# Optimization experiments

Measured on AMD Instinct MI355X. Metric: run time of the kernel, lower is better.

The kernel has to match this reference:

```python
import jax, jax.numpy as jnp
import numpy as np


def _filter_flow(img, filters, K):
    # img: [N, 2, H, W]; filters: [N, K*K, H, W] per-pixel adaptive kernels
    N, C, H, W = img.shape
    pad = (K - 1) // 2
    imgp = jnp.pad(img, ((0, 0), (0, 0), (pad, pad), (pad, pad)))
    # patches: [N, C*K*K, H, W], channel-major then row-major (dy, dx) --
    # matches torch F.unfold per single channel
    patches = jax.lax.conv_general_dilated_patches(
        imgp, (K, K), (1, 1), 'VALID',
        dimension_numbers=('NCHW', 'OIHW', 'NCHW'))
    patches = patches.reshape(N, C, K * K, H, W)
    return jnp.sum(patches * filters[:, None], axis=2)  # [N, 2, H, W]


def _grid(N, H, W, dtype):
    xx = jnp.broadcast_to(jnp.arange(W, dtype=dtype)[None, :], (H, W)) / max(W - 1, 1)
    yy = jnp.broadcast_to(jnp.arange(H, dtype=dtype)[:, None], (H, W)) / max(H - 1, 1)
    return jnp.broadcast_to(jnp.stack([xx, yy])[None], (N, 2, H, W))


def setup_inputs() -> dict:
    key = jax.random.key(0)
    k1, k2 = jax.random.split(key)
    N, K, H, W = 4, 11, 256, 256
    FF_AtoB = jax.random.uniform(k1, (N, K * K, H, W), dtype=jnp.float32)
    FF_BtoA = jax.random.uniform(k2, (N, K * K, H, W), dtype=jnp.float32)
    return {"FF_AtoB": FF_AtoB, "FF_BtoA": FF_BtoA, "filter_size": K}


def reference(FF_AtoB, FF_BtoA, filter_size):
    weight = 1.0
    N, C, H, W = FF_AtoB.shape
    K = filter_size
    grid = _grid(N, H, W, FF_AtoB.dtype)

    def cycle_loss(ff1, ff2):
        m = _filter_flow(grid, ff1, K)
        m = _filter_flow(m, ff2, K)
        diff = jnp.sqrt(jnp.sum((grid - m) ** 2, axis=1))  # [N, H, W]
        per_img = jnp.sum(diff, axis=(1, 2)) / (H * W)
        return jnp.sum(per_img) / N

    loss_ABA = cycle_loss(FF_AtoB, FF_BtoA)
    loss_BAB = cycle_loss(FF_BtoA, FF_AtoB)
    return (loss_ABA + loss_BAB) * weight
```

## Files before the change

kernel.cpp:

```cpp
#include <hip/hip_runtime.h>
#include <math.h>

#define NB   4
#define KF   11
#define KK   121
#define HH   256
#define WW   256
#define HW   (HH * WW)
#define PADK 5
#define TW   (WW + 2 * PADK)
#define INVD (1.0f / 255.0f)

__global__ __launch_bounds__(256) void pass1_kernel(const float* __restrict__ F,
                                                    float* __restrict__ m1) {
    const int n = blockIdx.x / HH;
    const int h = blockIdx.x % HH;
    const int w = threadIdx.x;

    const float* fp = F + (size_t)n * KK * HW + h * WW + w;

    float xv[KF], mk[KF];
#pragma unroll
    for (int kx = 0; kx < KF; ++kx) {
        int cc = w + kx - PADK;
        bool ok = (cc >= 0 && cc < WW);
        xv[kx] = ok ? (float)cc * INVD : 0.0f;
        mk[kx] = ok ? 1.0f : 0.0f;
    }

    float ax = 0.0f, ay = 0.0f;
    for (int ky = 0; ky < KF; ++ky) {
        int rr = h + ky - PADK;
        if (rr < 0 || rr >= HH) continue;
        float yv = (float)rr * INVD;
        const float* fr = fp + (size_t)ky * KF * HW;
        float srow = 0.0f;
#pragma unroll
        for (int kx = 0; kx < KF; ++kx) {
            float f = fr[(size_t)kx * HW];
            ax = fmaf(f, xv[kx], ax);
            srow = fmaf(f, mk[kx], srow);
        }
        ay = fmaf(yv, srow, ay);
    }

    size_t o = (size_t)n * 2 * HW + h * WW + w;
    m1[o] = ax;
    m1[o + HW] = ay;
}

template <bool FUSE>
__global__ __launch_bounds__(256) void pass2_kernel(const float* __restrict__ F,
                                                    const float* __restrict__ m1in,
                                                    float* __restrict__ m1out,
                                                    float* __restrict__ acc) {
    __shared__ float tile[2 * KF * TW];
    __shared__ float wsum[4];

    const int n = blockIdx.x / HH;
    const int h = blockIdx.x % HH;
    const int w = threadIdx.x;

    const float* mbase = m1in + (size_t)n * 2 * HW;
    for (int t = threadIdx.x; t < 2 * KF * TW; t += 256) {
        int ch = t / (KF * TW);
        int rem = t - ch * (KF * TW);
        int r = rem / TW;
        int c = rem - r * TW;
        int rr = h + r - PADK;
        int cc = c - PADK;
        float v = 0.0f;
        if (rr >= 0 && rr < HH && cc >= 0 && cc < WW)
            v = mbase[(size_t)ch * HW + rr * WW + cc];
        tile[t] = v;
    }
    __syncthreads();

    const float* fp = F + (size_t)n * KK * HW + h * WW + w;

    float xv[KF], mk[KF];
#pragma unroll
    for (int kx = 0; kx < KF; ++kx) {
        int cc = w + kx - PADK;
        bool ok = (cc >= 0 && cc < WW);
        xv[kx] = ok ? (float)cc * INVD : 0.0f;
        mk[kx] = ok ? 1.0f : 0.0f;
    }

    float a1x = 0.0f, a1y = 0.0f;
    float a2x = 0.0f, a2y = 0.0f;

    for (int ky = 0; ky < KF; ++ky) {
        int rr = h + ky - PADK;
        if (rr < 0 || rr >= HH) continue;
        float yv = (float)rr * INVD;
        const float* fr = fp + (size_t)ky * KF * HW;
        const float* t0 = tile + ky * TW + w;
        const float* t1 = t0 + KF * TW;
        float srow = 0.0f;
#pragma unroll
        for (int kx = 0; kx < KF; ++kx) {
            float f = fr[(size_t)kx * HW];
            if (FUSE) {
                a1x = fmaf(f, xv[kx], a1x);
                srow = fmaf(f, mk[kx], srow);
            }
            a2x = fmaf(f, t0[kx], a2x);
            a2y = fmaf(f, t1[kx], a2y);
        }
        if (FUSE) a1y = fmaf(yv, srow, a1y);
    }

    if (FUSE) {
        size_t o = (size_t)n * 2 * HW + h * WW + w;
        m1out[o] = a1x;
        m1out[o + HW] = a1y;
    }

    float gx = (float)w * INVD, gy = (float)h * INVD;
    float dx = gx - a2x, dy = gy - a2y;
    float d = sqrtf(dx * dx + dy * dy);

#pragma unroll
    for (int off = 32; off > 0; off >>= 1) d += __shfl_down(d, off, 64);
    int lane = threadIdx.x & 63, wid = threadIdx.x >> 6;
    if (lane == 0) wsum[wid] = d;
    __syncthreads();
    if (threadIdx.x == 0) atomicAdd(acc, wsum[0] + wsum[1] + wsum[2] + wsum[3]);
}

__global__ void finalize_kernel(const float* __restrict__ acc, float* __restrict__ out) {
    out[0] = (acc[0] + acc[1]) * (1.0f / ((float)HW * (float)NB));
}

extern "C" void kernel_launch(void* const* d_in, const int* in_sizes, int n_in,
                              void* d_out, int out_size, void* d_ws, size_t ws_size,
                              hipStream_t stream) {
    const float* FA = (const float*)d_in[0];
    const float* FB = (const float*)d_in[1];
    float* out = (float*)d_out;

    float* m1A = (float*)d_ws;
    float* m1B = m1A + (size_t)NB * 2 * HW;
    float* acc = m1B + (size_t)NB * 2 * HW;

    hipMemsetAsync(acc, 0, 2 * sizeof(float), stream);

    dim3 grid(NB * HH), block(256);
    pass1_kernel<<<grid, block, 0, stream>>>(FA, m1A);
    pass2_kernel<true><<<grid, block, 0, stream>>>(FB, m1A, m1B, acc);
    pass2_kernel<false><<<grid, block, 0, stream>>>(FA, m1B, nullptr, acc + 1);

    finalize_kernel<<<1, 1, 0, stream>>>(acc, out);
}
```

Baseline: 309.7 us.

## Process two pixels per thread and two rows per block with float2 loads

Each thread now computes two adjacent pixels using float2 loads of the filter planes, and each block covers two output rows, sharing one 12-row halo tile in shared memory. Tile values are loaded into registers once per row and reused across both pixels, so there are fewer LDS reads and wider global loads. Atomic accumulation is replaced by per-block partial sums that a 256-thread finalize kernel reduces, which also removes the memset. Register pressure goes up and the grid shrinks by half.

```diff
diff --git a/kernel.cpp b/kernel.cpp
--- a/kernel.cpp
+++ b/kernel.cpp
@@ -1,136 +1,179 @@
 #include <hip/hip_runtime.h>
 #include <math.h>
 
-#define NB   4
-#define KF   11
-#define KK   121
-#define HH   256
-#define WW   256
-#define HW   (HH * WW)
-#define PADK 5
-#define TW   (WW + 2 * PADK)
-#define INVD (1.0f / 255.0f)
+#define NB    4
+#define KF    11
+#define KK    121
+#define HH    256
+#define WW    256
+#define HW    (HH * WW)
+#define PADK  5
+#define TROWS 12
+#define TW2   268
+#define INVD  (1.0f / 255.0f)
+#define RPB   2
+#define GRID1 (NB * HH / RPB)
 
 __global__ __launch_bounds__(256) void pass1_kernel(const float* __restrict__ F,
                                                     float* __restrict__ m1) {
-    const int n = blockIdx.x / HH;
-    const int h = blockIdx.x % HH;
-    const int w = threadIdx.x;
+    const int t   = threadIdx.x;
+    const int n   = blockIdx.x / (HH / RPB);
+    const int h0  = (blockIdx.x % (HH / RPB)) * RPB;
+    const int sub = t >> 7;
+    const int j   = t & 127;
+    const int h   = h0 + sub;
+    const int w0  = j * 2;
 
-    const float* fp = F + (size_t)n * KK * HW + h * WW + w;
+    const float2* fp = (const float2*)(F + (size_t)n * KK * HW + (size_t)h * WW + w0);
 
-    float xv[KF], mk[KF];
+    float mk0[KF], mk1[KF];
 #pragma unroll
     for (int kx = 0; kx < KF; ++kx) {
-        int cc = w + kx - PADK;
-        bool ok = (cc >= 0 && cc < WW);
-        xv[kx] = ok ? (float)cc * INVD : 0.0f;
-        mk[kx] = ok ? 1.0f : 0.0f;
+        int c0 = w0 + kx - PADK;
+        mk0[kx] = (c0 >= 0 && c0 < WW) ? 1.0f : 0.0f;
+        mk1[kx] = (c0 + 1 >= 0 && c0 + 1 < WW) ? 1.0f : 0.0f;
     }
+    const float b0 = (float)(w0 - PADK) * INVD;
 
-    float ax = 0.0f, ay = 0.0f;
+    float ax0 = 0, ay0 = 0, ax1 = 0, ay1 = 0;
     for (int ky = 0; ky < KF; ++ky) {
         int rr = h + ky - PADK;
         if (rr < 0 || rr >= HH) continue;
         float yv = (float)rr * INVD;
-        const float* fr = fp + (size_t)ky * KF * HW;
-        float srow = 0.0f;
+        const float2* fr = fp + (size_t)(ky * KF) * (HW / 2);
+        float s0 = 0, s1 = 0;
 #pragma unroll
         for (int kx = 0; kx < KF; ++kx) {
-            float f = fr[(size_t)kx * HW];
-            ax = fmaf(f, xv[kx], ax);
-            srow = fmaf(f, mk[kx], srow);
+            float2 f = fr[(size_t)kx * (HW / 2)];
+            float u0 = f.x * mk0[kx], u1 = f.y * mk1[kx];
+            float xk = b0 + (float)kx * INVD;
+            ax0 = fmaf(u0, xk, ax0);
+            ax1 = fmaf(u1, xk + INVD, ax1);
+            s0 += u0; s1 += u1;
         }
-        ay = fmaf(yv, srow, ay);
+        ay0 = fmaf(yv, s0, ay0);
+        ay1 = fmaf(yv, s1, ay1);
     }
-
-    size_t o = (size_t)n * 2 * HW + h * WW + w;
-    m1[o] = ax;
-    m1[o + HW] = ay;
+    float2* ox = (float2*)(m1 + (size_t)n * 2 * HW + (size_t)h * WW + w0);
+    float2* oy = (float2*)(m1 + (size_t)n * 2 * HW + HW + (size_t)h * WW + w0);
+    *ox = make_float2(ax0, ax1);
+    *oy = make_float2(ay0, ay1);
 }
 
 template <bool FUSE>
 __global__ __launch_bounds__(256) void pass2_kernel(const float* __restrict__ F,
                                                     const float* __restrict__ m1in,
                                                     float* __restrict__ m1out,
-                                                    float* __restrict__ acc) {
-    __shared__ float tile[2 * KF * TW];
+                                                    float* __restrict__ partial) {
+    __shared__ float tile[2 * TROWS * TW2];
     __shared__ float wsum[4];
 
-    const int n = blockIdx.x / HH;
-    const int h = blockIdx.x % HH;
-    const int w = threadIdx.x;
+    const int t   = threadIdx.x;
+    const int n   = blockIdx.x / (HH / RPB);
+    const int h0  = (blockIdx.x % (HH / RPB)) * RPB;
+    const int sub = t >> 7;
+    const int j   = t & 127;
+    const int h   = h0 + sub;
+    const int w0  = j * 2;
 
     const float* mbase = m1in + (size_t)n * 2 * HW;
-    for (int t = threadIdx.x; t < 2 * KF * TW; t += 256) {
-        int ch = t / (KF * TW);
-        int rem = t - ch * (KF * TW);
-        int r = rem / TW;
-        int c = rem - r * TW;
-        int rr = h + r - PADK;
-        int cc = c - PADK;
+    for (int i = t; i < 2 * TROWS * TW2; i += 256) {
+        int ch  = i / (TROWS * TW2);
+        int rem = i - ch * (TROWS * TW2);
+        int r   = rem / TW2;
+        int c   = rem - r * TW2;
+        int rr  = h0 + r - PADK;
+        int cc  = c - PADK;
         float v = 0.0f;
         if (rr >= 0 && rr < HH && cc >= 0 && cc < WW)
             v = mbase[(size_t)ch * HW + rr * WW + cc];
-        tile[t] = v;
+        tile[i] = v;
     }
     __syncthreads();
 
-    const float* fp = F + (size_t)n * KK * HW + h * WW + w;
+    const float2* fp = (const float2*)(F + (size_t)n * KK * HW + (size_t)h * WW + w0);
 
-    float xv[KF], mk[KF];
+    float mk0[KF], mk1[KF];
 #pragma unroll
     for (int kx = 0; kx < KF; ++kx) {
-        int cc = w + kx - PADK;
-        bool ok = (cc >= 0 && cc < WW);
-        xv[kx] = ok ? (float)cc * INVD : 0.0f;
-        mk[kx] = ok ? 1.0f : 0.0f;
+        int c0 = w0 + kx - PADK;
+        mk0[kx] = (c0 >= 0 && c0 < WW) ? 1.0f : 0.0f;
+        mk1[kx] = (c0 + 1 >= 0 && c0 + 1 < WW) ? 1.0f : 0.0f;
     }
+    const float b0 = (float)(w0 - PADK) * INVD;
 
-    float a1x = 0.0f, a1y = 0.0f;
-    float a2x = 0.0f, a2y = 0.0f;
+    float a1x0 = 0, a1y0 = 0, a1x1 = 0, a1y1 = 0;
+    float a2x0 = 0, a2y0 = 0, a2x1 = 0, a2y1 = 0;
 
     for (int ky = 0; ky < KF; ++ky) {
         int rr = h + ky - PADK;
         if (rr < 0 || rr >= HH) continue;
         float yv = (float)rr * INVD;
-        const float* fr = fp + (size_t)ky * KF * HW;
-        const float* t0 = tile + ky * TW + w;
-        const float* t1 = t0 + KF * TW;
-        float srow = 0.0f;
+        const float2* fr = fp + (size_t)(ky * KF) * (HW / 2);
+
+        const float* tx = tile + (sub + ky) * TW2 + w0;
+        const float* ty = tx + TROWS * TW2;
+        float cx[12], cy[12];
+#pragma unroll
+        for (int q = 0; q < 6; ++q) {
+            float2 vx = *(const float2*)(tx + 2 * q);
+            float2 vy = *(const float2*)(ty + 2 * q);
+            cx[2 * q] = vx.x; cx[2 * q + 1] = vx.y;
+            cy[2 * q] = vy.x; cy[2 * q + 1] = vy.y;
+        }
+
+        float s0 = 0, s1 = 0;
 #pragma unroll
         for (int kx = 0; kx < KF; ++kx) {
-            float f = fr[(size_t)kx * HW];
+            float2 f = fr[(size_t)kx * (HW / 2)];
             if (FUSE) {
-                a1x = fmaf(f, xv[kx], a1x);
-                srow = fmaf(f, mk[kx], srow);
+                float u0 = f.x * mk0[kx], u1 = f.y * mk1[kx];
+                float xk = b0 + (float)kx * INVD;
+                a1x0 = fmaf(u0, xk, a1x0);
+                a1x1 = fmaf(u1, xk + INVD, a1x1);
+                s0 += u0; s1 += u1;
             }
-            a2x = fmaf(f, t0[kx], a2x);
-            a2y = fmaf(f, t1[kx], a2y);
+            a2x0 = fmaf(f.x, cx[kx], a2x0);
+            a2x1 = fmaf(f.y, cx[kx + 1], a2x1);
+            a2y0 = fmaf(f.x, cy[kx], a2y0);
+            a2y1 = fmaf(f.y, cy[kx + 1], a2y1);
         }
-        if (FUSE) a1y = fmaf(yv, srow, a1y);
+        if (FUSE) {
+            a1y0 = fmaf(yv, s0, a1y0);
+            a1y1 = fmaf(yv, s1, a1y1);
+        }
     }
 
     if (FUSE) {
-        size_t o = (size_t)n * 2 * HW + h * WW + w;
-        m1out[o] = a1x;
-        m1out[o + HW] = a1y;
+        float2* ox = (float2*)(m1out + (size_t)n * 2 * HW + (size_t)h * WW + w0);
+        float2* oy = (float2*)(m1out + (size_t)n * 2 * HW + HW + (size_t)h * WW + w0);
+        *ox = make_float2(a1x0, a1x1);
+        *oy = make_float2(a1y0, a1y1);
     }
 
-    float gx = (float)w * INVD, gy = (float)h * INVD;
-    float dx = gx - a2x, dy = gy - a2y;
-    float d = sqrtf(dx * dx + dy * dy);
+    float gx = (float)w0 * INVD, gy = (float)h * INVD;
+    float dx0 = gx - a2x0,        dy0 = gy - a2y0;
+    float dx1 = gx + INVD - a2x1, dy1 = gy - a2y1;
+    float d = sqrtf(dx0 * dx0 + dy0 * dy0) + sqrtf(dx1 * dx1 + dy1 * dy1);
 
 #pragma unroll
     for (int off = 32; off > 0; off >>= 1) d += __shfl_down(d, off, 64);
-    int lane = threadIdx.x & 63, wid = threadIdx.x >> 6;
-    if (lane == 0) wsum[wid] = d;
+    if ((t & 63) == 0) wsum[t >> 6] = d;
     __syncthreads();
-    if (threadIdx.x == 0) atomicAdd(acc, wsum[0] + wsum[1] + wsum[2] + wsum[3]);
+    if (t == 0) partial[blockIdx.x] = wsum[0] + wsum[1] + wsum[2] + wsum[3];
 }
 
-__global__ void finalize_kernel(const float* __restrict__ acc, float* __restrict__ out) {
-    out[0] = (acc[0] + acc[1]) * (1.0f / ((float)HW * (float)NB));
+__global__ __launch_bounds__(256) void finalize_kernel(const float* __restrict__ partial,
+                                                       float* __restrict__ out) {
+    __shared__ float wsum[4];
+    int t = threadIdx.x;
+    float s = partial[t] + partial[t + 256] + partial[t + 512] + partial[t + 768];
+#pragma unroll
+    for (int off = 32; off > 0; off >>= 1) s += __shfl_down(s, off, 64);
+    if ((t & 63) == 0) wsum[t >> 6] = s;
+    __syncthreads();
+    if (t == 0)
+        out[0] = (wsum[0] + wsum[1] + wsum[2] + wsum[3]) * (1.0f / ((float)HW * (float)NB));
 }
 
 extern "C" void kernel_launch(void* const* d_in, const int* in_sizes, int n_in,
@@ -142,14 +185,12 @@
 
     float* m1A = (float*)d_ws;
     float* m1B = m1A + (size_t)NB * 2 * HW;
-    float* acc = m1B + (size_t)NB * 2 * HW;
+    float* partial = m1B + (size_t)NB * 2 * HW;
 
-    hipMemsetAsync(acc, 0, 2 * sizeof(float), stream);
+    dim3 grid(GRID1), block(256);
+    pass1_kernel<<<grid, block, 0, stream>>>(FA, m1A);
+    pass2_kernel<true><<<grid, block, 0, stream>>>(FB, m1A, m1B, partial);
+    pass2_kernel<false><<<grid, block, 0, stream>>>(FA, m1B, nullptr, partial + GRID1);
 
-    dim3 grid(NB * HH), block(256);
-    pass1_kernel<<<grid, block, 0, stream>>>(FA, m1A);
-    pass2_kernel<true><<<grid, block, 0, stream>>>(FB, m1A, m1B, acc);
-    pass2_kernel<false><<<grid, block, 0, stream>>>(FA, m1B, nullptr, acc + 1);
-
-    finalize_kernel<<<1, 1, 0, stream>>>(acc, out);
+    finalize_kernel<<<1, block, 0, stream>>>(partial, out);
 }
```

After: 295.1 us. 4.7% less time.
